# Kernel tuning notes

Hardware: AMD Instinct MI355X
Metric: run time of the kernel (lower is better)

The kernel has to match this reference:

```python
import jax, jax.numpy as jnp
import numpy as np

N_NODES = 50000
N_EDGES = 800000
IN_CH, HID_CH, OUT_CH = 128, 128, 40


def setup_inputs() -> dict:
    key = jax.random.key(0)
    k1, k2, k3, k4 = jax.random.split(key, 4)
    x = jax.random.normal(k1, (N_NODES, IN_CH), dtype=jnp.float32)
    edge_index = jax.random.randint(k2, (2, N_EDGES), 0, N_NODES, dtype=jnp.int64)
    # Glorot-ish init for linear weights
    W1 = jax.random.normal(k3, (IN_CH, HID_CH), dtype=jnp.float32) / np.sqrt(IN_CH)
    b1 = jnp.zeros((HID_CH,), dtype=jnp.float32)
    W2 = jax.random.normal(k4, (HID_CH, OUT_CH), dtype=jnp.float32) / np.sqrt(HID_CH)
    b2 = jnp.zeros((OUT_CH,), dtype=jnp.float32)
    return {"x": x, "edge_index": edge_index, "W1": W1, "b1": b1, "W2": W2, "b2": b2}


def _gcn_conv(x, src, dst, W, b):
    # GCNConv(normalize=False): dense transform then sparse aggregation (scatter-add)
    h = x @ W                                   # [N, C_out]
    out = jax.ops.segment_sum(h[src], dst, num_segments=N_NODES)  # sum_{j->i} h[j]
    return out + b


def reference(x, edge_index, W1, b1, W2, b2):
    src, dst = edge_index[0], edge_index[1]
    h = _gcn_conv(x, src, dst, W1, b1)
    h = jax.nn.relu(h)
    # dropout is identity in eval mode
    h = _gcn_conv(h, src, dst, W2, b2)
    return jax.nn.log_softmax(h, axis=-1)
```

## Files before the change

### kernel.cpp

```cpp
#include <hip/hip_runtime.h>

#define NN 50000
#define NE 800000
#define NBKT 196
#define NBLK 256
#define EPB (NE / NBLK)
#define MATN (NBKT * NBLK)

using short8 = __attribute__((ext_vector_type(8))) short;
using f32x4  = __attribute__((ext_vector_type(4))) float;
union U4S8 { uint4 u; short8 v; };

__device__ __forceinline__ float lof(unsigned v) { return __uint_as_float(v << 16); }
__device__ __forceinline__ float hif(unsigned v) { return __uint_as_float(v & 0xffff0000u); }
__device__ __forceinline__ unsigned bf16rne(float f) {
    unsigned u = __float_as_uint(f);
    return (u + 0x7fffu + ((u >> 16) & 1u)) >> 16;
}
__device__ __forceinline__ unsigned pack2(float a, float b) {
    return bf16rne(a) | (bf16rne(b) << 16);
}
__device__ __forceinline__ unsigned fp8pack4(float a0, float a1, float a2, float a3) {
    int w = __builtin_amdgcn_cvt_pk_fp8_f32(a0, a1, 0, false);
    w = __builtin_amdgcn_cvt_pk_fp8_f32(a2, a3, w, true);
    return (unsigned)w;
}

__global__ __launch_bounds__(256) void binhist_k(const int* __restrict__ dst,
                                                 int* __restrict__ mat,
                                                 const float* __restrict__ W1,
                                                 const float* __restrict__ W2,
                                                 unsigned* __restrict__ W1T,
                                                 unsigned* __restrict__ W2T) {
    __shared__ int hist[NBKT];
    const int tid = threadIdx.x;
    for (int i = tid; i < NBKT; i += 256) hist[i] = 0;

    const int g = blockIdx.x * 256 + tid;
    if (g < 8192) {
        const int n = g >> 6, k2 = (g & 63) * 2;
        W1T[g] = pack2(W1[k2 * 128 + n], W1[(k2 + 1) * 128 + n]);
    } else if (g < 8192 + 3072) {
        const int u = g - 8192;
        const int n = u >> 6;
        const int q0 = (u & 63) * 2, q1 = q0 + 1;
        const int c0 = (q0 & 7) * 16 + (q0 >> 3);
        const int c1 = (q1 & 7) * 16 + (q1 >> 3);
        W2T[u] = (n < 40) ? pack2(W2[c0 * 40 + n], W2[c1 * 40 + n]) : 0u;
    }
    __syncthreads();

    const int base = blockIdx.x * EPB;
    for (int e = base + tid; e < base + EPB; e += 256)
        atomicAdd(&hist[dst[e] >> 8], 1);
    __syncthreads();
    for (int i = tid; i < NBKT; i += 256)
        mat[i * NBLK + blockIdx.x] = hist[i];
}

__global__ __launch_bounds__(256) void reduce_k(const int* __restrict__ mat,
                                                int* __restrict__ blocksum) {
    int v = mat[blockIdx.x * NBLK + threadIdx.x];
#pragma unroll
    for (int off = 32; off; off >>= 1) v += __shfl_xor(v, off, 64);
    __shared__ int ws[4];
    if ((threadIdx.x & 63) == 0) ws[threadIdx.x >> 6] = v;
    __syncthreads();
    if (threadIdx.x == 0) blocksum[blockIdx.x] = ws[0] + ws[1] + ws[2] + ws[3];
}

__global__ __launch_bounds__(256) void scanfin_k(int* __restrict__ mat,
                                                 const int* __restrict__ blocksum,
                                                 int* __restrict__ bucketoff) {
    __shared__ int bs[256];
    __shared__ int sm[256];
    const int t = threadIdx.x;
    const int b = blockIdx.x;
    const int mybs = (t < NBKT) ? blocksum[t] : 0;
    bs[t] = mybs;
    __syncthreads();
#pragma unroll
    for (int off = 1; off < 256; off <<= 1) {
        int u = (t >= off) ? bs[t - off] : 0;
        __syncthreads();
        bs[t] += u;
        __syncthreads();
    }
    if (b == 0) {
        if (t < NBKT) bucketoff[t] = bs[t] - mybs;
        if (t == 0) bucketoff[NBKT] = NE;
    }
    const int boff = bs[b] - blocksum[b];

    const int v = mat[b * NBLK + t];
    sm[t] = v;
    __syncthreads();
#pragma unroll
    for (int off = 1; off < 256; off <<= 1) {
        int u = (t >= off) ? sm[t - off] : 0;
        __syncthreads();
        sm[t] += u;
        __syncthreads();
    }
    mat[b * NBLK + t] = boff + sm[t] - v;
}

__global__ __launch_bounds__(256) void scatter_k(const int* __restrict__ src,
                                                 const int* __restrict__ dst,
                                                 const int* __restrict__ mat,
                                                 unsigned* __restrict__ binned) {
    __shared__ int cur[NBKT];
    const int tid = threadIdx.x;
    for (int i = tid; i < NBKT; i += 256) cur[i] = mat[i * NBLK + blockIdx.x];
    __syncthreads();
    const int base = blockIdx.x * EPB;
    for (int e = base + tid; e < base + EPB; e += 256) {
        const int d = dst[e];
        const int p = atomicAdd(&cur[d >> 8], 1);
        binned[p] = ((unsigned)(d & 255) << 16) | (unsigned)src[e];
    }
}

__global__ __launch_bounds__(256) void csrgemm1_k(const unsigned* __restrict__ binned,
                                                  const int* __restrict__ bucketoff,
                                                  int* __restrict__ rowoff,
                                                  unsigned short* __restrict__ eid,
                                                  const float* __restrict__ x,
                                                  const unsigned* __restrict__ W1T,
                                                  uint2* __restrict__ H1) {
    __shared__ int cnt[256];
    __shared__ int off[256];
    const int tid = threadIdx.x;
    if (blockIdx.x < NBKT) {
        const int b = blockIdx.x;
        const int beg = bucketoff[b];
        const int end = bucketoff[b + 1];
        cnt[tid] = 0;
        __syncthreads();
        for (int i = beg + tid; i < end; i += 256)
            atomicAdd(&cnt[(binned[i] >> 16) & 255u], 1);
        __syncthreads();
        const int v = cnt[tid];
        off[tid] = v;
        __syncthreads();
#pragma unroll
        for (int o = 1; o < 256; o <<= 1) {
            int u = (tid >= o) ? off[tid - o] : 0;
            __syncthreads();
            off[tid] += u;
            __syncthreads();
        }
        const int excl = off[tid] - v;
        const int node = b * 256 + tid;
        if (node <= NN) rowoff[node] = beg + excl;
        cnt[tid] = excl;
        __syncthreads();
        for (int i = beg + tid; i < end; i += 256) {
            const unsigned e = binned[i];
            const int p = atomicAdd(&cnt[(e >> 16) & 255u], 1);
            eid[beg + p] = (unsigned short)(e & 0xffffu);
        }
        return;
    }
    const int lane = tid & 63;
    const int cl = lane & 15;
    const int kh = lane >> 4;
    const int gw = ((blockIdx.x - NBKT) * 256 + tid) >> 6;

    short8 Bf[8][4];
#pragma unroll
    for (int c = 0; c < 8; ++c)
#pragma unroll
        for (int kc = 0; kc < 4; ++kc) {
            U4S8 tb;
            tb.u = *(const uint4*)(W1T + ((c * 16 + cl) * 128 + kc * 32 + kh * 8) / 2);
            Bf[c][kc] = tb.v;
        }

    for (int mt = gw; mt < 3125; mt += 1024) {
        const int r0 = mt * 16;
        const float* ap = x + (long)(r0 + cl) * 128 + kh * 8;
        f32x4 acc[8];
#pragma unroll
        for (int c = 0; c < 8; ++c) acc[c] = (f32x4){0.f, 0.f, 0.f, 0.f};
#pragma unroll
        for (int kc = 0; kc < 4; ++kc) {
            const float4 p0 = *(const float4*)(ap + kc * 32);
            const float4 p1 = *(const float4*)(ap + kc * 32 + 4);
            U4S8 af;
            af.u.x = pack2(p0.x, p0.y);
            af.u.y = pack2(p0.z, p0.w);
            af.u.z = pack2(p1.x, p1.y);
            af.u.w = pack2(p1.z, p1.w);
#pragma unroll
            for (int c = 0; c < 8; ++c)
                acc[c] = __builtin_amdgcn_mfma_f32_16x16x32_bf16(af.v, Bf[c][kc], acc[c], 0, 0, 0);
        }
#pragma unroll
        for (int j = 0; j < 4; ++j) {
            uint2 o;
            o.x = fp8pack4(acc[0][j], acc[1][j], acc[2][j], acc[3][j]);
            o.y = fp8pack4(acc[4][j], acc[5][j], acc[6][j], acc[7][j]);
            H1[(long)(r0 + kh * 4 + j) * 16 + cl] = o;
        }
    }
}

__global__ __launch_bounds__(256) void gather1_k(const uint4* __restrict__ H1,
                                                 const int* __restrict__ rowoff,
                                                 const unsigned short* __restrict__ eid,
                                                 const float* __restrict__ b1,
                                                 uint4* __restrict__ h) {
    const int n = blockIdx.x * 4 + (threadIdx.x >> 6);
    const int lane = threadIdx.x & 63;
    const int g = lane >> 3;
    const int cl = lane & 7;
    const int beg = rowoff[n], end = rowoff[n + 1];
    float a[16];
#pragma unroll
    for (int i = 0; i < 16; ++i) a[i] = 0.f;

#define ACC16(v)                                                             \
    {                                                                        \
        auto t0 = __builtin_amdgcn_cvt_pk_f32_fp8((int)(v).x, false);        \
        auto t1 = __builtin_amdgcn_cvt_pk_f32_fp8((int)(v).x, true);         \
        auto t2 = __builtin_amdgcn_cvt_pk_f32_fp8((int)(v).y, false);        \
        auto t3 = __builtin_amdgcn_cvt_pk_f32_fp8((int)(v).y, true);         \
        auto t4 = __builtin_amdgcn_cvt_pk_f32_fp8((int)(v).z, false);        \
        auto t5 = __builtin_amdgcn_cvt_pk_f32_fp8((int)(v).z, true);         \
        auto t6 = __builtin_amdgcn_cvt_pk_f32_fp8((int)(v).w, false);        \
        auto t7 = __builtin_amdgcn_cvt_pk_f32_fp8((int)(v).w, true);         \
        a[0] += t0[0];  a[1] += t0[1];  a[2] += t1[0];  a[3] += t1[1];       \
        a[4] += t2[0];  a[5] += t2[1];  a[6] += t3[0];  a[7] += t3[1];       \
        a[8] += t4[0];  a[9] += t4[1];  a[10] += t5[0]; a[11] += t5[1];      \
        a[12] += t6[0]; a[13] += t6[1]; a[14] += t7[0]; a[15] += t7[1];      \
    }

    int k = beg;
    for (; k + 15 < end; k += 16) {
        const uint4 vA = H1[eid[k + g] * 8 + cl];
        const uint4 vB = H1[eid[k + 8 + g] * 8 + cl];
        ACC16(vA);
        ACC16(vB);
    }
    for (; k + 7 < end; k += 8) {
        const uint4 v = H1[eid[k + g] * 8 + cl];
        ACC16(v);
    }
    if (k + g < end) {
        const uint4 v = H1[eid[k + g] * 8 + cl];
        ACC16(v);
    }
#undef ACC16

#pragma unroll
    for (int i = 0; i < 16; ++i) {
        a[i] += __shfl_xor(a[i], 8, 64);
        a[i] += __shfl_xor(a[i], 16, 64);
        a[i] += __shfl_xor(a[i], 32, 64);
    }
    if (lane < 8) {
        float r[16];
#pragma unroll
        for (int i = 0; i < 16; ++i)
            r[i] = fmaxf(a[i] + b1[(i & 7) * 16 + cl * 2 + (i >> 3)], 0.f);
        uint4 o1, o2;
        o1.x = pack2(r[0], r[1]);  o1.y = pack2(r[2], r[3]);
        o1.z = pack2(r[4], r[5]);  o1.w = pack2(r[6], r[7]);
        o2.x = pack2(r[8], r[9]);  o2.y = pack2(r[10], r[11]);
        o2.z = pack2(r[12], r[13]); o2.w = pack2(r[14], r[15]);
        h[n * 16 + cl * 2] = o1;
        h[n * 16 + cl * 2 + 1] = o2;
    }
}

__global__ __launch_bounds__(256) void gemm2_k(const unsigned* __restrict__ h,
                                               const unsigned* __restrict__ W2T,
                                               unsigned* __restrict__ H2) {
    const int lane = threadIdx.x & 63;
    const int cl = lane & 15;
    const int kh = lane >> 4;
    const int gw = (blockIdx.x * 256 + threadIdx.x) >> 6;

    short8 Bf[3][4];
#pragma unroll
    for (int c = 0; c < 3; ++c)
#pragma unroll
        for (int kc = 0; kc < 4; ++kc) {
            U4S8 tb;
            tb.u = *(const uint4*)(W2T + ((c * 16 + cl) * 128 + kc * 32 + kh * 8) / 2);
            Bf[c][kc] = tb.v;
        }

    for (int mt = gw; mt < 3125; mt += 1024) {
        const int r0 = mt * 16;
        const unsigned* ap = h + (long)(r0 + cl) * 64 + kh * 4;
        f32x4 acc[3];
#pragma unroll
        for (int c = 0; c < 3; ++c) acc[c] = (f32x4){0.f, 0.f, 0.f, 0.f};
#pragma unroll
        for (int kc = 0; kc < 4; ++kc) {
            U4S8 af;
            af.u = *(const uint4*)(ap + kc * 16);
#pragma unroll
            for (int c = 0; c < 3; ++c)
                acc[c] = __builtin_amdgcn_mfma_f32_16x16x32_bf16(af.v, Bf[c][kc], acc[c], 0, 0, 0);
        }
#pragma unroll
        for (int j = 0; j < 4; ++j)
            H2[(long)(r0 + kh * 4 + j) * 16 + cl] =
                fp8pack4(acc[0][j], acc[1][j], acc[2][j], 0.f);
    }
}

__global__ __launch_bounds__(256) void gather2_k(const unsigned* __restrict__ H2,
                                                 const int* __restrict__ rowoff,
                                                 const unsigned short* __restrict__ eid,
                                                 const float* __restrict__ b2,
                                                 float* __restrict__ out) {
    const int n = blockIdx.x * 4 + (threadIdx.x >> 6);
    const int lane = threadIdx.x & 63;
    const int g = lane >> 4;
    const int q = lane & 15;
    const int beg = rowoff[n], end = rowoff[n + 1];
    float a0 = 0.f, a1 = 0.f, a2 = 0.f;

#define ACCQ(u)                                                              \
    {                                                                        \
        auto t0 = __builtin_amdgcn_cvt_pk_f32_fp8((int)(u), false);          \
        auto t1 = __builtin_amdgcn_cvt_pk_f32_fp8((int)(u), true);           \
        a0 += t0[0]; a1 += t0[1]; a2 += t1[0];                               \
    }

    int k = beg;
    for (; k + 7 < end; k += 8) {
        const unsigned uA = H2[eid[k + g] * 16 + q];
        const unsigned uB = H2[eid[k + 4 + g] * 16 + q];
        ACCQ(uA);
        ACCQ(uB);
    }
    for (; k + 3 < end; k += 4) {
        const unsigned u = H2[eid[k + g] * 16 + q];
        ACCQ(u);
    }
    if (k + g < end) {
        const unsigned u = H2[eid[k + g] * 16 + q];
        ACCQ(u);
    }
#undef ACCQ

    a0 += __shfl_xor(a0, 16, 64); a0 += __shfl_xor(a0, 32, 64);
    a1 += __shfl_xor(a1, 16, 64); a1 += __shfl_xor(a1, 32, 64);
    a2 += __shfl_xor(a2, 16, 64); a2 += __shfl_xor(a2, 32, 64);

    const bool has2 = (q < 8);
    const float v0 = a0 + b2[q];
    const float v1 = a1 + b2[16 + q];
    const float v2 = has2 ? (a2 + b2[32 + q]) : -INFINITY;
    float m = fmaxf(fmaxf(v0, v1), v2);
#pragma unroll
    for (int off = 8; off; off >>= 1) m = fmaxf(m, __shfl_xor(m, off, 64));
    float e = expf(v0 - m) + expf(v1 - m) + (has2 ? expf(v2 - m) : 0.f);
#pragma unroll
    for (int off = 8; off; off >>= 1) e += __shfl_xor(e, off, 64);
    const float ls = logf(e);
    if (lane < 16) {
        float* op = out + (long)n * 40;
        op[q] = v0 - m - ls;
        op[16 + q] = v1 - m - ls;
        if (has2) op[32 + q] = v2 - m - ls;
    }
}

extern "C" void kernel_launch(void* const* d_in, const int* in_sizes, int n_in,
                              void* d_out, int out_size, void* d_ws, size_t ws_size,
                              hipStream_t stream) {
    const float* x  = (const float*)d_in[0];
    const int*   ei = (const int*)d_in[1];
    const float* W1 = (const float*)d_in[2];
    const float* b1 = (const float*)d_in[3];
    const float* W2 = (const float*)d_in[4];
    const float* b2 = (const float*)d_in[5];
    const int* src = ei;
    const int* dst = ei + NE;

    unsigned* H1   = (unsigned*)d_ws;
    unsigned* h    = H1 + (size_t)NN * 32;
    unsigned* H2   = h + (size_t)NN * 64;
    unsigned* W1T  = H2 + (size_t)NN * 16;
    unsigned* W2T  = W1T + 8192;
    int* mat       = (int*)(W2T + 3072);
    int* blocksum  = mat + MATN;
    int* bucketoff = blocksum + 256;
    int* rowoff    = bucketoff + NBKT + 1;
    unsigned short* eid = (unsigned short*)(rowoff + NN + 1);
    unsigned* binned = h;
    float* out     = (float*)d_out;

    binhist_k<<<NBLK, 256, 0, stream>>>(dst, mat, W1, W2, W1T, W2T);
    reduce_k<<<NBKT, 256, 0, stream>>>(mat, blocksum);
    scanfin_k<<<NBKT, 256, 0, stream>>>(mat, blocksum, bucketoff);
    scatter_k<<<NBLK, 256, 0, stream>>>(src, dst, mat, binned);
    csrgemm1_k<<<NBKT + 256, 256, 0, stream>>>(binned, bucketoff, rowoff, eid,
                                               x, W1T, (uint2*)H1);
    gather1_k<<<12500, 256, 0, stream>>>((const uint4*)H1, rowoff, eid, b1, (uint4*)h);
    gemm2_k<<<256, 256, 0, stream>>>(h, W2T, H2);
    gather2_k<<<12500, 256, 0, stream>>>(H2, rowoff, eid, b2, out);
}
```

Measured before the change: 103.7 us.

## Fuse layer-1 gather with layer-2 GEMM through shared memory

```diff
diff --git a/kernel.cpp b/kernel.cpp
--- a/kernel.cpp
+++ b/kernel.cpp
@@ -11,8 +11,6 @@
 using f32x4  = __attribute__((ext_vector_type(4))) float;
 union U4S8 { uint4 u; short8 v; };
 
-__device__ __forceinline__ float lof(unsigned v) { return __uint_as_float(v << 16); }
-__device__ __forceinline__ float hif(unsigned v) { return __uint_as_float(v & 0xffff0000u); }
 __device__ __forceinline__ unsigned bf16rne(float f) {
     unsigned u = __float_as_uint(f);
     return (u + 0x7fffu + ((u >> 16) & 1u)) >> 16;
@@ -206,19 +204,20 @@
     }
 }
 
-__global__ __launch_bounds__(256) void gather1_k(const uint4* __restrict__ H1,
-                                                 const int* __restrict__ rowoff,
-                                                 const unsigned short* __restrict__ eid,
-                                                 const float* __restrict__ b1,
-                                                 uint4* __restrict__ h) {
-    const int n = blockIdx.x * 4 + (threadIdx.x >> 6);
-    const int lane = threadIdx.x & 63;
+#define HLSTRIDE 68
+__global__ __launch_bounds__(256) void g1g2_k(const uint4* __restrict__ H1,
+                                              const int* __restrict__ rowoff,
+                                              const unsigned short* __restrict__ eid,
+                                              const float* __restrict__ b1,
+                                              const unsigned* __restrict__ W2T,
+                                              unsigned* __restrict__ H2) {
+    __shared__ unsigned hl[16 * HLSTRIDE];
+    const int tid = threadIdx.x;
+    const int w = tid >> 6;
+    const int lane = tid & 63;
     const int g = lane >> 3;
-    const int cl = lane & 7;
-    const int beg = rowoff[n], end = rowoff[n + 1];
-    float a[16];
-#pragma unroll
-    for (int i = 0; i < 16; ++i) a[i] = 0.f;
+    const int cl8 = lane & 7;
+    const int n0 = blockIdx.x * 16;
 
 #define ACC16(v)                                                             \
     {                                                                        \
@@ -236,79 +235,80 @@
         a[12] += t6[0]; a[13] += t6[1]; a[14] += t7[0]; a[15] += t7[1];      \
     }
 
-    int k = beg;
-    for (; k + 15 < end; k += 16) {
-        const uint4 vA = H1[eid[k + g] * 8 + cl];
-        const uint4 vB = H1[eid[k + 8 + g] * 8 + cl];
-        ACC16(vA);
-        ACC16(vB);
-    }
-    for (; k + 7 < end; k += 8) {
-        const uint4 v = H1[eid[k + g] * 8 + cl];
-        ACC16(v);
-    }
-    if (k + g < end) {
-        const uint4 v = H1[eid[k + g] * 8 + cl];
-        ACC16(v);
+#pragma unroll 1
+    for (int i = 0; i < 4; ++i) {
+        const int r = w * 4 + i;
+        const int n = n0 + r;
+        const int beg = rowoff[n], end = rowoff[n + 1];
+        float a[16];
+#pragma unroll
+        for (int j = 0; j < 16; ++j) a[j] = 0.f;
+
+        int k = beg;
+        for (; k + 15 < end; k += 16) {
+            const uint4 vA = H1[eid[k + g] * 8 + cl8];
+            const uint4 vB = H1[eid[k + 8 + g] * 8 + cl8];
+            ACC16(vA);
+            ACC16(vB);
+        }
+        for (; k + 7 < end; k += 8) {
+            const uint4 v = H1[eid[k + g] * 8 + cl8];
+            ACC16(v);
+        }
+        if (k + g < end) {
+            const uint4 v = H1[eid[k + g] * 8 + cl8];
+            ACC16(v);
+        }
+
+#pragma unroll
+        for (int j = 0; j < 16; ++j) {
+            a[j] += __shfl_xor(a[j], 8, 64);
+            a[j] += __shfl_xor(a[j], 16, 64);
+            a[j] += __shfl_xor(a[j], 32, 64);
+        }
+        if (lane < 8) {
+            float rr[16];
+#pragma unroll
+            for (int j = 0; j < 16; ++j)
+                rr[j] = fmaxf(a[j] + b1[(j & 7) * 16 + cl8 * 2 + (j >> 3)], 0.f);
+            uint4 o1, o2;
+            o1.x = pack2(rr[0], rr[1]);   o1.y = pack2(rr[2], rr[3]);
+            o1.z = pack2(rr[4], rr[5]);   o1.w = pack2(rr[6], rr[7]);
+            o2.x = pack2(rr[8], rr[9]);   o2.y = pack2(rr[10], rr[11]);
+            o2.z = pack2(rr[12], rr[13]); o2.w = pack2(rr[14], rr[15]);
+            *(uint4*)&hl[r * HLSTRIDE + cl8 * 8] = o1;
+            *(uint4*)&hl[r * HLSTRIDE + cl8 * 8 + 4] = o2;
+        }
     }
 #undef ACC16
-
-#pragma unroll
-    for (int i = 0; i < 16; ++i) {
-        a[i] += __shfl_xor(a[i], 8, 64);
-        a[i] += __shfl_xor(a[i], 16, 64);
-        a[i] += __shfl_xor(a[i], 32, 64);
-    }
-    if (lane < 8) {
-        float r[16];
-#pragma unroll
-        for (int i = 0; i < 16; ++i)
-            r[i] = fmaxf(a[i] + b1[(i & 7) * 16 + cl * 2 + (i >> 3)], 0.f);
-        uint4 o1, o2;
-        o1.x = pack2(r[0], r[1]);  o1.y = pack2(r[2], r[3]);
-        o1.z = pack2(r[4], r[5]);  o1.w = pack2(r[6], r[7]);
-        o2.x = pack2(r[8], r[9]);  o2.y = pack2(r[10], r[11]);
-        o2.z = pack2(r[12], r[13]); o2.w = pack2(r[14], r[15]);
-        h[n * 16 + cl * 2] = o1;
-        h[n * 16 + cl * 2 + 1] = o2;
-    }
-}
-
-__global__ __launch_bounds__(256) void gemm2_k(const unsigned* __restrict__ h,
-                                               const unsigned* __restrict__ W2T,
-                                               unsigned* __restrict__ H2) {
-    const int lane = threadIdx.x & 63;
-    const int cl = lane & 15;
-    const int kh = lane >> 4;
-    const int gw = (blockIdx.x * 256 + threadIdx.x) >> 6;
-
-    short8 Bf[3][4];
-#pragma unroll
-    for (int c = 0; c < 3; ++c)
-#pragma unroll
-        for (int kc = 0; kc < 4; ++kc) {
-            U4S8 tb;
-            tb.u = *(const uint4*)(W2T + ((c * 16 + cl) * 128 + kc * 32 + kh * 8) / 2);
-            Bf[c][kc] = tb.v;
-        }
-
-    for (int mt = gw; mt < 3125; mt += 1024) {
-        const int r0 = mt * 16;
-        const unsigned* ap = h + (long)(r0 + cl) * 64 + kh * 4;
+    __syncthreads();
+
+    if (w == 0) {
+        const int cl = lane & 15;
+        const int kh = lane >> 4;
+        short8 Bf[3][4];
+#pragma unroll
+        for (int c = 0; c < 3; ++c)
+#pragma unroll
+            for (int kc = 0; kc < 4; ++kc) {
+                U4S8 tb;
+                tb.u = *(const uint4*)(W2T + ((c * 16 + cl) * 128 + kc * 32 + kh * 8) / 2);
+                Bf[c][kc] = tb.v;
+            }
         f32x4 acc[3];
 #pragma unroll
         for (int c = 0; c < 3; ++c) acc[c] = (f32x4){0.f, 0.f, 0.f, 0.f};
 #pragma unroll
         for (int kc = 0; kc < 4; ++kc) {
             U4S8 af;
-            af.u = *(const uint4*)(ap + kc * 16);
+            af.u = *(const uint4*)&hl[cl * HLSTRIDE + kh * 4 + kc * 16];
 #pragma unroll
             for (int c = 0; c < 3; ++c)
                 acc[c] = __builtin_amdgcn_mfma_f32_16x16x32_bf16(af.v, Bf[c][kc], acc[c], 0, 0, 0);
         }
 #pragma unroll
         for (int j = 0; j < 4; ++j)
-            H2[(long)(r0 + kh * 4 + j) * 16 + cl] =
+            H2[(long)(n0 + kh * 4 + j) * 16 + cl] =
                 fp8pack4(acc[0][j], acc[1][j], acc[2][j], 0.f);
     }
 }
@@ -385,8 +385,7 @@
     const int* dst = ei + NE;
 
     unsigned* H1   = (unsigned*)d_ws;
-    unsigned* h    = H1 + (size_t)NN * 32;
-    unsigned* H2   = h + (size_t)NN * 64;
+    unsigned* H2   = H1 + (size_t)NN * 32;
     unsigned* W1T  = H2 + (size_t)NN * 16;
     unsigned* W2T  = W1T + 8192;
     int* mat       = (int*)(W2T + 3072);
@@ -394,7 +393,7 @@
     int* bucketoff = blocksum + 256;
     int* rowoff    = bucketoff + NBKT + 1;
     unsigned short* eid = (unsigned short*)(rowoff + NN + 1);
-    unsigned* binned = h;
+    unsigned* binned = (unsigned*)(eid + NE);
     float* out     = (float*)d_out;
 
     binhist_k<<<NBLK, 256, 0, stream>>>(dst, mat, W1, W2, W1T, W2T);
@@ -403,7 +402,6 @@
     scatter_k<<<NBLK, 256, 0, stream>>>(src, dst, mat, binned);
     csrgemm1_k<<<NBKT + 256, 256, 0, stream>>>(binned, bucketoff, rowoff, eid,
                                                x, W1T, (uint2*)H1);
-    gather1_k<<<12500, 256, 0, stream>>>((const uint4*)H1, rowoff, eid, b1, (uint4*)h);
-    gemm2_k<<<256, 256, 0, stream>>>(h, W2T, H2);
+    g1g2_k<<<3125, 256, 0, stream>>>((const uint4*)H1, rowoff, eid, b1, W2T, H2);
     gather2_k<<<12500, 256, 0, stream>>>(H2, rowoff, eid, b2, out);
 }
```

After: 107.9 us. 4.0% more time.
